# Optimization experiments

Hardware: AMD Instinct MI355X
Metric: run time of the kernel (lower is better)

Reference implementation:

```python
import jax, jax.numpy as jnp
import numpy as np

HEADS = 2

def gat_layer(x, edge_index, W, att, bias):
    # x: [N, Fin], W: [H*C, Fin], att: [1, H, 2C], bias: [C]
    N = x.shape[0]
    C = bias.shape[0]
    # add self loops (source_to_target: x_j from row 0, aggregate onto row 1)
    loop = jnp.arange(N, dtype=edge_index.dtype)
    src = jnp.concatenate([edge_index[0], loop])
    dst = jnp.concatenate([edge_index[1], loop])
    h = (x @ W.T).reshape(N, HEADS, C)          # [N, H, C]
    x_j = h[src]                                 # [E, H, C]
    x_i = h[dst]                                 # [E, H, C]
    x_cat = jnp.concatenate([x_i, x_j], axis=-1) # [E, H, 2C]
    alpha = (x_cat * att).sum(-1)                # [E, H]
    alpha = jnp.where(alpha >= 0, alpha, 0.2 * alpha)  # leaky_relu(0.2)
    # NOTE: module uses a global (not per-destination) normalization
    alpha = jnp.exp(alpha - alpha.max())
    alpha = alpha / (alpha.sum(axis=0, keepdims=True) + 1e-10)
    msg = x_j * alpha[..., None]                 # [E, H, C]
    aggr = jax.ops.segment_sum(msg, dst, num_segments=N)  # [N, H, C]
    return aggr.mean(axis=1) + bias              # [N, C]

def setup_inputs() -> dict:
    key = jax.random.key(0)
    ks = jax.random.split(key, 7)
    N, Fin, C = 50000, 128, 64
    E = 800000
    x = jax.random.normal(ks[0], (N, Fin), dtype=jnp.float32)
    edge_index = jax.random.randint(ks[1], (2, E), 0, N, dtype=jnp.int64)
    W1 = jax.random.normal(ks[2], (HEADS * C, Fin), dtype=jnp.float32) * 0.05
    att1 = jax.random.normal(ks[3], (1, HEADS, 2 * C), dtype=jnp.float32) * 0.05
    b1 = jnp.zeros((C,), dtype=jnp.float32)
    W2 = jax.random.normal(ks[4], (HEADS * C, C), dtype=jnp.float32) * 0.05
    att2 = jax.random.normal(ks[5], (1, HEADS, 2 * C), dtype=jnp.float32) * 0.05
    b2 = jnp.zeros((C,), dtype=jnp.float32)
    return {"x": x, "edge_index": edge_index, "W1": W1, "att1": att1,
            "b1": b1, "W2": W2, "att2": att2, "b2": b2}

def reference(x, edge_index, W1, att1, b1, W2, att2, b2):
    h = gat_layer(x, edge_index, W1, att1, b1)
    h = jax.nn.relu(h)
    # F.dropout with training flag: treated as eval (identity) for determinism
    out = gat_layer(h, edge_index, W2, att2, b2)
    return out
```

## Files before the change

kernel.cpp:

```cpp
#include <hip/hip_runtime.h>
#include <hip/hip_bf16.h>
#include <math.h>


#define HP 8
#define HG 64
#define NHISTB (HP * HG)
#define HRANGE_MAX 6272
#define NSELF 16
#define NWGT  256

using short8 = __attribute__((ext_vector_type(8))) short;
using f32x4  = __attribute__((ext_vector_type(4))) float;

__device__ __forceinline__ unsigned f2bf(float x) {
  unsigned u = __float_as_uint(x);
  return (u + 0x7fffu + ((u >> 16) & 1u)) >> 16;
}
__device__ __forceinline__ float bflo(unsigned p) { return __uint_as_float(p << 16); }
__device__ __forceinline__ float bfhi(unsigned p) { return __uint_as_float(p & 0xffff0000u); }
__device__ __forceinline__ float lrexp(float a) {
  a = a >= 0.f ? a : 0.2f * a;
  return __expf(a);
}

__device__ __forceinline__ void block_zadd(float z0, float z1,
                                           float* __restrict__ Zp) {
  __shared__ float r0[16], r1[16];
  int lane = threadIdx.x & 63, w = threadIdx.x >> 6;
  int nw = blockDim.x >> 6;
#pragma unroll
  for (int off = 32; off; off >>= 1) {
    z0 += __shfl_down(z0, off, 64);
    z1 += __shfl_down(z1, off, 64);
  }
  if (lane == 0) { r0[w] = z0; r1[w] = z1; }
  __syncthreads();
  if (threadIdx.x == 0) {
    float s0 = 0.f, s1 = 0.f;
    for (int i = 0; i < nw; ++i) { s0 += r0[i]; s1 += r1[i]; }
    atomicAdd(&Zp[0], s0);
    atomicAdd(&Zp[1], s1);
  }
}

__global__ __launch_bounds__(256) void init_ws(
    const float* __restrict__ W1, const float* __restrict__ W2,
    unsigned short* __restrict__ wbf1, unsigned short* __restrict__ wbf2,
    float* __restrict__ Z) {
  int tid = blockIdx.x * 256 + threadIdx.x;
  int stride = gridDim.x * 256;
  for (int i = tid; i < 128 * 128; i += stride)
    wbf1[i] = (unsigned short)f2bf(W1[i]);
  for (int i = tid; i < 128 * 64; i += stride)
    wbf2[i] = (unsigned short)f2bf(W2[i]);
  if (tid < 4) Z[tid] = 0.f;
}

template <int FIN>
__global__ __launch_bounds__(256) void gemm_mfma(
    const float* __restrict__ x, const unsigned short* __restrict__ Wb,
    const float* __restrict__ att, unsigned* __restrict__ hq,
    float* __restrict__ si, float* __restrict__ sj,
    int N,
    const int* __restrict__ dstE, int* __restrict__ partial,
    int E, int nhistb, int hstep, int eper) {
  const int tid = threadIdx.x;

  constexpr int WB = 128 * FIN * 2;
  constexpr int SMEM = (WB > HRANGE_MAX * 4) ? WB : HRANGE_MAX * 4;
  __shared__ __align__(16) unsigned char smem[SMEM];

  if ((int)blockIdx.x < nhistb) {
    int* lhist = (int*)smem;
    const int p = blockIdx.x & (HP - 1);
    const int g = blockIdx.x >> 3;
    const int lo = p * hstep;
    for (int i = tid; i < hstep; i += 256) lhist[i] = 0;
    __syncthreads();
    const int eb = g * eper;
    const int ee = min(E, eb + eper);
    int e = eb + tid;
    for (; e + 3 * 256 < ee; e += 4 * 256) {
      int d0 = dstE[e] - lo;
      int d1 = dstE[e + 256] - lo;
      int d2 = dstE[e + 2 * 256] - lo;
      int d3 = dstE[e + 3 * 256] - lo;
      if ((unsigned)d0 < (unsigned)hstep) atomicAdd(&lhist[d0], 1);
      if ((unsigned)d1 < (unsigned)hstep) atomicAdd(&lhist[d1], 1);
      if ((unsigned)d2 < (unsigned)hstep) atomicAdd(&lhist[d2], 1);
      if ((unsigned)d3 < (unsigned)hstep) atomicAdd(&lhist[d3], 1);
    }
    for (; e < ee; e += 256) {
      int d = dstE[e] - lo;
      if ((unsigned)d < (unsigned)hstep) atomicAdd(&lhist[d], 1);
    }
    __syncthreads();
    for (int i = tid; i < hstep; i += 256) {
      int node = lo + i;
      if (node < N) partial[(size_t)g * N + node] = lhist[i];
    }
    return;
  }

  constexpr int KS = FIN / 32;
  constexpr int CPR = FIN / 8;
  constexpr int NCHUNK = 128 * CPR;

  unsigned short* wlds = (unsigned short*)smem;

  const int w    = tid >> 6;
  const int lane = tid & 63;
  const int cl   = lane & 15;
  const int grp  = lane >> 4;
  const int n0   = (blockIdx.x - nhistb) * 64;

  const int arow = n0 + w * 16 + cl;
  const bool avalid = arow < N;
  float4 av0[KS], av1[KS];
#pragma unroll
  for (int ks = 0; ks < KS; ++ks) {
    av0[ks] = make_float4(0.f, 0.f, 0.f, 0.f);
    av1[ks] = av0[ks];
    if (avalid) {
      const float4* xp =
          (const float4*)(x + (size_t)arow * FIN + ks * 32 + grp * 8);
      av0[ks] = xp[0];
      av1[ks] = xp[1];
    }
  }

  const uint4* Wb4 = (const uint4*)Wb;
  for (int c = tid; c < NCHUNK; c += 256) {
    int row = c / CPR;
    int cc  = c & (CPR - 1);
    *(uint4*)&wlds[row * FIN + ((cc ^ (row & (CPR - 1))) * 8)] = Wb4[c];
  }
  __syncthreads();

  short8 afrag[KS];
#pragma unroll
  for (int ks = 0; ks < KS; ++ks) {
    union { short8 s8; unsigned u[4]; } af;
    af.u[0] = f2bf(av0[ks].x) | (f2bf(av0[ks].y) << 16);
    af.u[1] = f2bf(av0[ks].z) | (f2bf(av0[ks].w) << 16);
    af.u[2] = f2bf(av1[ks].x) | (f2bf(av1[ks].y) << 16);
    af.u[3] = f2bf(av1[ks].z) | (f2bf(av1[ks].w) << 16);
    afrag[ks] = af.s8;
  }

  f32x4 acc[8];
#pragma unroll
  for (int ct = 0; ct < 8; ++ct) acc[ct] = (f32x4){0.f, 0.f, 0.f, 0.f};

  const int swz = cl & (CPR - 1);
#pragma unroll
  for (int ks = 0; ks < KS; ++ks) {
#pragma unroll
    for (int ct = 0; ct < 8; ++ct) {
      const unsigned short* bp =
          &wlds[(ct * 16 + cl) * FIN + (((ks * 4 + grp) ^ swz) * 8)];
      short8 bfrag = *(const short8*)bp;
      acc[ct] = __builtin_amdgcn_mfma_f32_16x16x32_bf16(afrag[ks], bfrag,
                                                        acc[ct], 0, 0, 0);
    }
  }

  float ai[8], aj[8];
#pragma unroll
  for (int ct = 0; ct < 8; ++ct) {
    int hd = ct >> 2;
    int cw = (ct & 3) * 16 + cl;
    ai[ct] = att[hd * 128 + cw];
    aj[ct] = att[hd * 128 + 64 + cw];
  }

#pragma unroll
  for (int r = 0; r < 4; ++r) {
    int node = n0 + w * 16 + grp * 4 + r;
    float s0i = 0.f, s0j = 0.f, s1i = 0.f, s1j = 0.f;
    unsigned wpk[4];
#pragma unroll
    for (int ct = 0; ct < 4; ++ct) {
      float v0 = acc[ct][r];
      float v1 = acc[ct + 4][r];
      s0i += v0 * ai[ct];
      s0j += v0 * aj[ct];
      s1i += v1 * ai[ct + 4];
      s1j += v1 * aj[ct + 4];
      wpk[ct] = f2bf(v0) | (f2bf(v1) << 16);
    }
#pragma unroll
    for (int off = 8; off; off >>= 1) {
      s0i += __shfl_xor(s0i, off, 64);
      s0j += __shfl_xor(s0j, off, 64);
      s1i += __shfl_xor(s1i, off, 64);
      s1j += __shfl_xor(s1j, off, 64);
    }
    if (node < N) {
#pragma unroll
      for (int ct = 0; ct < 4; ++ct)
        hq[(size_t)node * 64 + ct * 16 + cl] = wpk[ct];
      if (cl == 0) {
        si[node * 2 + 0] = s0i;
        si[node * 2 + 1] = s1i;
        sj[node * 2 + 0] = s0j;
        sj[node * 2 + 1] = s1j;
      }
    }
  }
}

__global__ __launch_bounds__(256) void scan_blocks(
    const int* __restrict__ partial, int* __restrict__ rowptr,
    int* __restrict__ bsum, int N) {
  __shared__ int ts[256];
  int b = blockIdx.x, t = threadIdx.x;
  int base = b * 1024 + t * 4;
  int s0 = 0, s1 = 0, s2 = 0, s3 = 0;
  if (base < N) {
    const int4* p4 = (const int4*)partial;
#pragma unroll 4
    for (int g = 0; g < HG; ++g) {
      int4 v = p4[((size_t)g * N + base) >> 2];
      s0 += v.x; s1 += v.y; s2 += v.z; s3 += v.w;
    }
  }
  int v[4] = {s0, s1, s2, s3};
  int tot = s0 + s1 + s2 + s3;
  ts[t] = tot;
  __syncthreads();
#pragma unroll
  for (int off = 1; off < 256; off <<= 1) {
    int x = (t >= off) ? ts[t - off] : 0;
    __syncthreads();
    ts[t] += x;
    __syncthreads();
  }
  int run = ts[t] - tot;
#pragma unroll
  for (int j = 0; j < 4; ++j) {
    if (base + j < N) rowptr[base + j] = run;
    run += v[j];
  }
  if (t == 255) bsum[b] = ts[255];
}

__global__ __launch_bounds__(256) void scan_finish(
    int* __restrict__ rowptr, const int* __restrict__ bsum,
    int* __restrict__ partial, int N, int Eall, int nb) {
  __shared__ int pre[256];
  if (threadIdx.x == 0) {
    int run = 0;
    for (int i = 0; i < nb; ++i) { pre[i] = run; run += bsum[i]; }
  }
  __syncthreads();
  int tid = blockIdx.x * blockDim.x + threadIdx.x;
  int stride = gridDim.x * blockDim.x;
  for (int i = tid; i < N; i += stride) {
    int v = rowptr[i] + pre[i >> 10];
    rowptr[i] = v;
    int run = v;
#pragma unroll 8
    for (int g = 0; g < HG; ++g) {
      int c = partial[(size_t)g * N + i];
      partial[(size_t)g * N + i] = run;
      run += c;
    }
  }
  if (tid == 0) rowptr[N] = Eall;
}

__global__ __launch_bounds__(1024) void scatter_z(
    const int* __restrict__ srcE, const int* __restrict__ dstE,
    const int* __restrict__ partial, float4* __restrict__ erec,
    const float2* __restrict__ si2, const float2* __restrict__ sj2,
    float* __restrict__ Zp, int E, int hstep, int N, int eper) {
  __shared__ __align__(16) int lcur[HRANGE_MAX];
  const int tid = threadIdx.x;
  float z0 = 0.f, z1 = 0.f;

  if ((int)blockIdx.x < NSELF) {
    for (int n = blockIdx.x * 1024 + tid; n < N; n += NSELF * 1024) {
      float2 a = si2[n], b = sj2[n];
      z0 += lrexp(a.x + b.x);
      z1 += lrexp(a.y + b.y);
    }
    block_zadd(z0, z1, Zp);
    return;
  }

  const int bid = blockIdx.x - NSELF;
  const int p = bid & (HP - 1);
  const int g = bid >> 3;
  const int lo = p * hstep;
  for (int i = tid; i < hstep; i += 1024) {
    int node = lo + i;
    lcur[i] = (node < N) ? partial[(size_t)g * N + node] : 0;
  }
  __syncthreads();

  const int eb = g * eper;
  const int ee = min(E, eb + eper);
  int e = eb + tid;
  for (; e + 3 * 1024 < ee; e += 4 * 1024) {
    int d0 = dstE[e], d1 = dstE[e + 1024];
    int d2 = dstE[e + 2 * 1024], d3 = dstE[e + 3 * 1024];
    int s0 = srcE[e], s1 = srcE[e + 1024];
    int s2 = srcE[e + 2 * 1024], s3 = srcE[e + 3 * 1024];
    int t0 = d0 - lo, t1 = d1 - lo, t2 = d2 - lo, t3 = d3 - lo;
    if ((unsigned)t0 < (unsigned)hstep) {
      float2 siv = si2[d0], sjv = sj2[s0];
      float w0 = lrexp(siv.x + sjv.x), w1 = lrexp(siv.y + sjv.y);
      z0 += w0; z1 += w1;
      erec[atomicAdd(&lcur[t0], 1)] =
          make_float4(__int_as_float(s0), __int_as_float(d0), w0, w1);
    }
    if ((unsigned)t1 < (unsigned)hstep) {
      float2 siv = si2[d1], sjv = sj2[s1];
      float w0 = lrexp(siv.x + sjv.x), w1 = lrexp(siv.y + sjv.y);
      z0 += w0; z1 += w1;
      erec[atomicAdd(&lcur[t1], 1)] =
          make_float4(__int_as_float(s1), __int_as_float(d1), w0, w1);
    }
    if ((unsigned)t2 < (unsigned)hstep) {
      float2 siv = si2[d2], sjv = sj2[s2];
      float w0 = lrexp(siv.x + sjv.x), w1 = lrexp(siv.y + sjv.y);
      z0 += w0; z1 += w1;
      erec[atomicAdd(&lcur[t2], 1)] =
          make_float4(__int_as_float(s2), __int_as_float(d2), w0, w1);
    }
    if ((unsigned)t3 < (unsigned)hstep) {
      float2 siv = si2[d3], sjv = sj2[s3];
      float w0 = lrexp(siv.x + sjv.x), w1 = lrexp(siv.y + sjv.y);
      z0 += w0; z1 += w1;
      erec[atomicAdd(&lcur[t3], 1)] =
          make_float4(__int_as_float(s3), __int_as_float(d3), w0, w1);
    }
  }
  for (; e < ee; e += 1024) {
    int d = dstE[e];
    int dd = d - lo;
    if ((unsigned)dd < (unsigned)hstep) {
      int s = srcE[e];
      float2 siv = si2[d], sjv = sj2[s];
      float w0 = lrexp(siv.x + sjv.x), w1 = lrexp(siv.y + sjv.y);
      z0 += w0; z1 += w1;
      erec[atomicAdd(&lcur[dd], 1)] =
          make_float4(__int_as_float(s), __int_as_float(d), w0, w1);
    }
  }
  block_zadd(z0, z1, Zp);
}

__global__ __launch_bounds__(1024) void z_wgt2(
    const float2* __restrict__ si2, const float2* __restrict__ sj2,
    float* __restrict__ Zp, float4* __restrict__ erec, int E, int N) {
  const int tid = threadIdx.x;
  float z0 = 0.f, z1 = 0.f;
  if ((int)blockIdx.x < NSELF) {
    for (int n = blockIdx.x * 1024 + tid; n < N; n += NSELF * 1024) {
      float2 a = si2[n], b = sj2[n];
      z0 += lrexp(a.x + b.x);
      z1 += lrexp(a.y + b.y);
    }
  } else {
    int k = (blockIdx.x - NSELF) * 1024 + tid;
    for (; k < E; k += NWGT * 1024) {
      float4 r = erec[k];
      int s = __float_as_int(r.x);
      int d = __float_as_int(r.y);
      float2 siv = si2[d];
      float2 sjv = sj2[s];
      r.z = lrexp(siv.x + sjv.x);
      r.w = lrexp(siv.y + sjv.y);
      z0 += r.z; z1 += r.w;
      erec[k] = r;
    }
  }
  block_zadd(z0, z1, Zp);
}

__device__ __forceinline__ void edge4r(
    const float4* __restrict__ erec, int k, const unsigned* __restrict__ hq,
    int lane, float& acc0, float& acc1) {
  float4 r0 = erec[k], r1 = erec[k + 1], r2 = erec[k + 2], r3 = erec[k + 3];
  unsigned p0 = hq[(size_t)__float_as_int(r0.x) * 64 + lane];
  unsigned p1 = hq[(size_t)__float_as_int(r1.x) * 64 + lane];
  unsigned p2 = hq[(size_t)__float_as_int(r2.x) * 64 + lane];
  unsigned p3 = hq[(size_t)__float_as_int(r3.x) * 64 + lane];
  acc0 = fmaf(bflo(p0), r0.z, acc0);
  acc1 = fmaf(bfhi(p0), r0.w, acc1);
  acc0 = fmaf(bflo(p1), r1.z, acc0);
  acc1 = fmaf(bfhi(p1), r1.w, acc1);
  acc0 = fmaf(bflo(p2), r2.z, acc0);
  acc1 = fmaf(bfhi(p2), r2.w, acc1);
  acc0 = fmaf(bflo(p3), r3.z, acc0);
  acc1 = fmaf(bfhi(p3), r3.w, acc1);
}
__device__ __forceinline__ void edge1r(
    int s, float w0, float w1, const unsigned* __restrict__ hq, int lane,
    float& acc0, float& acc1) {
  unsigned p = hq[(size_t)s * 64 + lane];
  acc0 = fmaf(bflo(p), w0, acc0);
  acc1 = fmaf(bfhi(p), w1, acc1);
}

__global__ __launch_bounds__(256) void csr_aggregate(
    const int* __restrict__ rowptr, const float4* __restrict__ erec,
    const unsigned* __restrict__ hq, const float2* __restrict__ si2,
    const float2* __restrict__ sj2, const float* __restrict__ Zp,
    const float* __restrict__ bias, float* __restrict__ out,
    int N, int do_relu) {
  int lane = threadIdx.x & 63;
  int wid = (blockIdx.x * blockDim.x + threadIdx.x) >> 6;
  int nw = (gridDim.x * blockDim.x) >> 6;
  float z0 = 1.f / (Zp[0] + 1e-10f);
  float z1 = 1.f / (Zp[1] + 1e-10f);
  float bv = bias[lane];
  for (int n0 = wid; n0 < N; n0 += nw) {
    int n = __builtin_amdgcn_readfirstlane(n0);
    int beg = rowptr[n], end = rowptr[n + 1];
    float2 siv = si2[n];
    float2 jv = sj2[n];
    float acc0 = 0.f, acc1 = 0.f;
    edge1r(n, lrexp(siv.x + jv.x), lrexp(siv.y + jv.y), hq, lane, acc0, acc1);
    int k = beg;
    for (; k + 4 <= end; k += 4) edge4r(erec, k, hq, lane, acc0, acc1);
    for (; k < end; ++k) {
      float4 r = erec[k];
      edge1r(__float_as_int(r.x), r.z, r.w, hq, lane, acc0, acc1);
    }
    float r = 0.5f * (acc0 * z0 + acc1 * z1) + bv;
    if (do_relu) r = fmaxf(r, 0.f);
    out[(size_t)n * 64 + lane] = r;
  }
}

extern "C" void kernel_launch(void* const* d_in, const int* in_sizes, int n_in,
                              void* d_out, int out_size, void* d_ws, size_t ws_size,
                              hipStream_t stream) {
  const float* x    = (const float*)d_in[0];
  const int*   ei   = (const int*)d_in[1];
  const float* W1   = (const float*)d_in[2];
  const float* att1 = (const float*)d_in[3];
  const float* b1   = (const float*)d_in[4];
  const float* W2   = (const float*)d_in[5];
  const float* att2 = (const float*)d_in[6];
  const float* b2   = (const float*)d_in[7];
  float* out = (float*)d_out;

  const int N = in_sizes[0] / 128;
  const int E = in_sizes[1] / 2;
  const int* srcE = ei;
  const int* dstE = ei + E;

  unsigned* hq = (unsigned*)d_ws;
  float* si    = (float*)(hq + (size_t)N * 64);
  float* sj    = si + (size_t)N * 2;
  float* Z     = sj + (size_t)N * 2;
  float* x2    = Z + 4;
  int* partial = (int*)x2;
  int* rowptr  = (int*)(x2 + (size_t)N * 64);
  int* bsum    = rowptr + (N + 1);
  uintptr_t ep = ((uintptr_t)(bsum + 256) + 15) & ~(uintptr_t)15;
  float4* erec = (float4*)ep;
  unsigned short* wbf1 = (unsigned short*)(erec + E);
  unsigned short* wbf2 = wbf1 + 128 * 128;

  dim3 blk(256);
  dim3 blk1k(1024);
  int nb = (N + 1023) / 1024;
  int ntiles = (N + 63) / 64;
  int hstep = (N + HP - 1) / HP;
  int eper  = (E + HG - 1) / HG;

  init_ws<<<64, blk, 0, stream>>>(W1, W2, wbf1, wbf2, Z);
  gemm_mfma<128><<<NHISTB + ntiles, blk, 0, stream>>>(
      x, wbf1, att1, hq, si, sj, N, dstE, partial, E, NHISTB, hstep, eper);
  scan_blocks<<<nb, blk, 0, stream>>>(partial, rowptr, bsum, N);
  scan_finish<<<256, blk, 0, stream>>>(rowptr, bsum, partial, N, E, nb);
  scatter_z<<<NSELF + NHISTB, blk1k, 0, stream>>>(
      srcE, dstE, partial, erec, (const float2*)si, (const float2*)sj,
      Z, E, hstep, N, eper);
  csr_aggregate<<<4096, blk, 0, stream>>>(rowptr, erec, hq,
                                          (const float2*)si, (const float2*)sj,
                                          Z, b1, x2, N, 1);
  gemm_mfma<64><<<ntiles, blk, 0, stream>>>(
      x2, wbf2, att2, hq, si, sj, N, dstE, partial, E, 0, hstep, eper);
  z_wgt2<<<NSELF + NWGT, blk1k, 0, stream>>>(
      (const float2*)si, (const float2*)sj, Z + 2, erec, E, N);
  csr_aggregate<<<4096, blk, 0, stream>>>(rowptr, erec, hq,
                                          (const float2*)si, (const float2*)sj,
                                          Z + 2, b2, out, N, 0);
}
```

Baseline: 256.3 us.

## Store per-group histogram offsets as uint16 and unroll CSR gather by eight

```diff
diff --git a/kernel.cpp b/kernel.cpp
--- a/kernel.cpp
+++ b/kernel.cpp
@@ -63,7 +63,7 @@
     const float* __restrict__ att, unsigned* __restrict__ hq,
     float* __restrict__ si, float* __restrict__ sj,
     int N,
-    const int* __restrict__ dstE, int* __restrict__ partial,
+    const int* __restrict__ dstE, unsigned short* __restrict__ partial,
     int E, int nhistb, int hstep, int eper) {
   const int tid = threadIdx.x;
 
@@ -98,7 +98,7 @@
     __syncthreads();
     for (int i = tid; i < hstep; i += 256) {
       int node = lo + i;
-      if (node < N) partial[(size_t)g * N + node] = lhist[i];
+      if (node < N) partial[(size_t)g * N + node] = (unsigned short)lhist[i];
     }
     return;
   }
@@ -212,18 +212,21 @@
 }
 
 __global__ __launch_bounds__(256) void scan_blocks(
-    const int* __restrict__ partial, int* __restrict__ rowptr,
+    const unsigned short* __restrict__ partial, int* __restrict__ rowptr,
     int* __restrict__ bsum, int N) {
   __shared__ int ts[256];
   int b = blockIdx.x, t = threadIdx.x;
   int base = b * 1024 + t * 4;
   int s0 = 0, s1 = 0, s2 = 0, s3 = 0;
   if (base < N) {
-    const int4* p4 = (const int4*)partial;
 #pragma unroll 4
     for (int g = 0; g < HG; ++g) {
-      int4 v = p4[((size_t)g * N + base) >> 2];
-      s0 += v.x; s1 += v.y; s2 += v.z; s3 += v.w;
+      unsigned long long v =
+          *(const unsigned long long*)&partial[(size_t)g * N + base];
+      s0 += (int)(v & 0xffffu);
+      s1 += (int)((v >> 16) & 0xffffu);
+      s2 += (int)((v >> 32) & 0xffffu);
+      s3 += (int)((v >> 48) & 0xffffu);
     }
   }
   int v[4] = {s0, s1, s2, s3};
@@ -248,7 +251,7 @@
 
 __global__ __launch_bounds__(256) void scan_finish(
     int* __restrict__ rowptr, const int* __restrict__ bsum,
-    int* __restrict__ partial, int N, int Eall, int nb) {
+    unsigned short* __restrict__ partial, int N, int Eall, int nb) {
   __shared__ int pre[256];
   if (threadIdx.x == 0) {
     int run = 0;
@@ -260,11 +263,11 @@
   for (int i = tid; i < N; i += stride) {
     int v = rowptr[i] + pre[i >> 10];
     rowptr[i] = v;
-    int run = v;
+    int run = 0;
 #pragma unroll 8
     for (int g = 0; g < HG; ++g) {
       int c = partial[(size_t)g * N + i];
-      partial[(size_t)g * N + i] = run;
+      partial[(size_t)g * N + i] = (unsigned short)run;
       run += c;
     }
   }
@@ -273,7 +276,8 @@
 
 __global__ __launch_bounds__(1024) void scatter_z(
     const int* __restrict__ srcE, const int* __restrict__ dstE,
-    const int* __restrict__ partial, float4* __restrict__ erec,
+    const unsigned short* __restrict__ partial, const int* __restrict__ rowptr,
+    float4* __restrict__ erec,
     const float2* __restrict__ si2, const float2* __restrict__ sj2,
     float* __restrict__ Zp, int E, int hstep, int N, int eper) {
   __shared__ __align__(16) int lcur[HRANGE_MAX];
@@ -296,7 +300,9 @@
   const int lo = p * hstep;
   for (int i = tid; i < hstep; i += 1024) {
     int node = lo + i;
-    lcur[i] = (node < N) ? partial[(size_t)g * N + node] : 0;
+    lcur[i] = (node < N)
+                  ? rowptr[node] + (int)partial[(size_t)g * N + node]
+                  : 0;
   }
   __syncthreads();
 
@@ -381,6 +387,28 @@
   block_zadd(z0, z1, Zp);
 }
 
+__device__ __forceinline__ void edge8r(
+    const float4* __restrict__ erec, int k, const unsigned* __restrict__ hq,
+    int lane, float& acc0, float& acc1) {
+  float4 r0 = erec[k],     r1 = erec[k + 1], r2 = erec[k + 2], r3 = erec[k + 3];
+  float4 r4 = erec[k + 4], r5 = erec[k + 5], r6 = erec[k + 6], r7 = erec[k + 7];
+  unsigned p0 = hq[(size_t)__float_as_int(r0.x) * 64 + lane];
+  unsigned p1 = hq[(size_t)__float_as_int(r1.x) * 64 + lane];
+  unsigned p2 = hq[(size_t)__float_as_int(r2.x) * 64 + lane];
+  unsigned p3 = hq[(size_t)__float_as_int(r3.x) * 64 + lane];
+  unsigned p4 = hq[(size_t)__float_as_int(r4.x) * 64 + lane];
+  unsigned p5 = hq[(size_t)__float_as_int(r5.x) * 64 + lane];
+  unsigned p6 = hq[(size_t)__float_as_int(r6.x) * 64 + lane];
+  unsigned p7 = hq[(size_t)__float_as_int(r7.x) * 64 + lane];
+  acc0 = fmaf(bflo(p0), r0.z, acc0);  acc1 = fmaf(bfhi(p0), r0.w, acc1);
+  acc0 = fmaf(bflo(p1), r1.z, acc0);  acc1 = fmaf(bfhi(p1), r1.w, acc1);
+  acc0 = fmaf(bflo(p2), r2.z, acc0);  acc1 = fmaf(bfhi(p2), r2.w, acc1);
+  acc0 = fmaf(bflo(p3), r3.z, acc0);  acc1 = fmaf(bfhi(p3), r3.w, acc1);
+  acc0 = fmaf(bflo(p4), r4.z, acc0);  acc1 = fmaf(bfhi(p4), r4.w, acc1);
+  acc0 = fmaf(bflo(p5), r5.z, acc0);  acc1 = fmaf(bfhi(p5), r5.w, acc1);
+  acc0 = fmaf(bflo(p6), r6.z, acc0);  acc1 = fmaf(bfhi(p6), r6.w, acc1);
+  acc0 = fmaf(bflo(p7), r7.z, acc0);  acc1 = fmaf(bfhi(p7), r7.w, acc1);
+}
 __device__ __forceinline__ void edge4r(
     const float4* __restrict__ erec, int k, const unsigned* __restrict__ hq,
     int lane, float& acc0, float& acc1) {
@@ -389,14 +417,10 @@
   unsigned p1 = hq[(size_t)__float_as_int(r1.x) * 64 + lane];
   unsigned p2 = hq[(size_t)__float_as_int(r2.x) * 64 + lane];
   unsigned p3 = hq[(size_t)__float_as_int(r3.x) * 64 + lane];
-  acc0 = fmaf(bflo(p0), r0.z, acc0);
-  acc1 = fmaf(bfhi(p0), r0.w, acc1);
-  acc0 = fmaf(bflo(p1), r1.z, acc0);
-  acc1 = fmaf(bfhi(p1), r1.w, acc1);
-  acc0 = fmaf(bflo(p2), r2.z, acc0);
-  acc1 = fmaf(bfhi(p2), r2.w, acc1);
-  acc0 = fmaf(bflo(p3), r3.z, acc0);
-  acc1 = fmaf(bfhi(p3), r3.w, acc1);
+  acc0 = fmaf(bflo(p0), r0.z, acc0);  acc1 = fmaf(bfhi(p0), r0.w, acc1);
+  acc0 = fmaf(bflo(p1), r1.z, acc0);  acc1 = fmaf(bfhi(p1), r1.w, acc1);
+  acc0 = fmaf(bflo(p2), r2.z, acc0);  acc1 = fmaf(bfhi(p2), r2.w, acc1);
+  acc0 = fmaf(bflo(p3), r3.z, acc0);  acc1 = fmaf(bfhi(p3), r3.w, acc1);
 }
 __device__ __forceinline__ void edge1r(
     int s, float w0, float w1, const unsigned* __restrict__ hq, int lane,
@@ -426,7 +450,8 @@
     float acc0 = 0.f, acc1 = 0.f;
     edge1r(n, lrexp(siv.x + jv.x), lrexp(siv.y + jv.y), hq, lane, acc0, acc1);
     int k = beg;
-    for (; k + 4 <= end; k += 4) edge4r(erec, k, hq, lane, acc0, acc1);
+    for (; k + 8 <= end; k += 8) edge8r(erec, k, hq, lane, acc0, acc1);
+    if (k + 4 <= end) { edge4r(erec, k, hq, lane, acc0, acc1); k += 4; }
     for (; k < end; ++k) {
       float4 r = erec[k];
       edge1r(__float_as_int(r.x), r.z, r.w, hq, lane, acc0, acc1);
@@ -460,7 +485,7 @@
   float* sj    = si + (size_t)N * 2;
   float* Z     = sj + (size_t)N * 2;
   float* x2    = Z + 4;
-  int* partial = (int*)x2;
+  unsigned short* partial = (unsigned short*)x2;
   int* rowptr  = (int*)(x2 + (size_t)N * 64);
   int* bsum    = rowptr + (N + 1);
   uintptr_t ep = ((uintptr_t)(bsum + 256) + 15) & ~(uintptr_t)15;
@@ -481,8 +506,8 @@
   scan_blocks<<<nb, blk, 0, stream>>>(partial, rowptr, bsum, N);
   scan_finish<<<256, blk, 0, stream>>>(rowptr, bsum, partial, N, E, nb);
   scatter_z<<<NSELF + NHISTB, blk1k, 0, stream>>>(
-      srcE, dstE, partial, erec, (const float2*)si, (const float2*)sj,
-      Z, E, hstep, N, eper);
+      srcE, dstE, partial, rowptr, erec, (const float2*)si,
+      (const float2*)sj, Z, E, hstep, N, eper);
   csr_aggregate<<<4096, blk, 0, stream>>>(rowptr, erec, hq,
                                           (const float2*)si, (const float2*)sj,
                                           Z, b1, x2, N, 1);
```

Measured after the change: 247.9 us. 3.3% less time.
